# Kernel optimization log

Hardware: AMD Instinct MI355X
Metric: run time of the kernel (lower is better)

The kernel has to match this reference:

```python
import jax, jax.numpy as jnp
import numpy as np

EPS_SLOPE = 1e-4
EPS_AVG = 1e-8
MIN_AVG = 1e-6
EPS_SCALE = 1e-3


def _slopes_yk(xk, delta_raw):
    # xk: [D, K] sorted knot x-positions; delta_raw: [D, K-1]
    seg_dx = xk[:, 1:] - xk[:, :-1]                      # [D, K-1]
    slopes = jax.nn.softplus(delta_raw) + EPS_SLOPE       # [D, K-1]
    avg = (slopes * seg_dx).sum(1, keepdims=True) / (seg_dx.sum(1, keepdims=True) + EPS_AVG)
    avg = jnp.maximum(avg, MIN_AVG)
    slopes = slopes / avg
    yk = jnp.concatenate(
        [jnp.zeros((xk.shape[0], 1), dtype=xk.dtype), jnp.cumsum(slopes * seg_dx, axis=1)],
        axis=1,
    )                                                     # [D, K]
    return slopes, yk


def setup_inputs() -> dict:
    key = jax.random.key(0)
    k1, k2, k3, k4, k5 = jax.random.split(key, 5)
    N, D, K = 1_000_000, 64, 32
    x = jax.random.normal(k1, (N, D), dtype=jnp.float32)
    # sorted knots per dim, spanning roughly the data range
    xk = jnp.sort(jax.random.normal(k2, (D, K), dtype=jnp.float32) * 2.0, axis=1)
    delta_raw = jax.random.normal(k3, (D, K - 1), dtype=jnp.float32) * 0.1
    scale_raw = jax.random.normal(k4, (D,), dtype=jnp.float32) * 0.1
    shift = jax.random.normal(k5, (D,), dtype=jnp.float32) * 0.1
    return {"x": x, "xk": xk, "delta_raw": delta_raw, "scale_raw": scale_raw, "shift": shift}


def reference(x, xk, delta_raw, scale_raw, shift):
    # x: [N, D]; xk: [D, K]
    D, K = xk.shape
    slopes, yk = _slopes_yk(xk, delta_raw)
    xT = x.T                                              # [D, N]
    # per-dim binary search (torch.searchsorted default == side='left')
    idx = jax.vmap(lambda knots, vals: jnp.searchsorted(knots, vals))(xk, xT)
    i0 = jnp.clip(idx, 1, K - 1) - 1                      # [D, N]
    x0 = jnp.take_along_axis(xk, i0, axis=1)              # [D, N]
    y0 = jnp.take_along_axis(yk, i0, axis=1)
    m = jnp.take_along_axis(slopes, i0, axis=1)
    y = (y0 + m * (xT - x0)).T                            # [N, D]
    scale = jax.nn.softplus(scale_raw) + EPS_SCALE
    return y * scale + shift
```

## Files before the change

### kernel.cpp

```cpp
#include <hip/hip_runtime.h>
#include <math.h>

#define D 64
#define KNOTS 32
#define NSEG 31
#define G 512
#define TSTR 66

typedef float f2v __attribute__((ext_vector_type(2)));

__device__ __forceinline__ float softplus_f(float v) {
  return fmaxf(v, 0.f) + log1pf(expf(-fabsf(v)));
}

__global__ __launch_bounds__(1024, 8) void pwl_fused(
    const float* __restrict__ x, const float* __restrict__ xk,
    const float* __restrict__ delta_raw, const float* __restrict__ scale_raw,
    const float* __restrict__ shift, float* __restrict__ out, int nrows) {
  __shared__ float kL[KNOTS * D];
  __shared__ float2 sAB[NSEG * D];
  __shared__ unsigned char tab[G * TSTR];
  __shared__ float invS[D], nloS[D];

  const int tid = threadIdx.x;

  for (int i = tid; i < D * KNOTS; i += blockDim.x) {
    int d = i >> 5, j = i & 31;
    int sd = (d >> 1) | ((d & 1) << 5);
    kL[j * D + sd] = xk[i];
  }
  __syncthreads();

  if (tid < D) {
    const int sd = tid;
    const int d = ((sd & 31) << 1) | (sd >> 5);
    float num = 0.f, den = 0.f;
    for (int s = 0; s < NSEG; ++s) {
      float sp = softplus_f(delta_raw[d * NSEG + s]) + 1e-4f;
      float dx = kL[(s + 1) * D + sd] - kL[s * D + sd];
      num += sp * dx;
      den += dx;
    }
    float avg = fmaxf(num / (den + 1e-8f), 1e-6f);
    float scale = softplus_f(scale_raw[d]) + 1e-3f;
    float sh = shift[d];
    float y = 0.f;
    for (int s = 0; s < NSEG; ++s) {
      float sp = softplus_f(delta_raw[d * NSEG + s]) + 1e-4f;
      float m = sp / avg;
      float k0 = kL[s * D + sd];
      sAB[s * D + sd] = make_float2(m * scale, (y - m * k0) * scale + sh);
      y += m * (kL[(s + 1) * D + sd] - k0);
    }
    float lo = kL[1 * D + sd];
    float hi = kL[(KNOTS - 1) * D + sd];
    float inv = (float)G / (hi - lo);
    invS[sd] = inv;
    nloS[sd] = -lo * inv;
  }
  __syncthreads();

  for (int p = tid; p < G * D; p += blockDim.x) {
    const int sd = p & 63;
    const int c = p >> 6;
    const float inv = invS[sd], nlo = nloS[sd];
    int b = 0;
#pragma unroll
    for (int half = 16; half > 0; half >>= 1) {
      float kv = kL[(b + half) * D + sd];
      float cf = fminf(fmaxf(fmaf(kv, inv, nlo), 0.f), (float)(G - 1));
      b += ((int)cf < c) ? half : 0;
    }
    tab[c * TSTR + sd] = (unsigned char)min(b, 30);
  }
  __syncthreads();

  const int lane = tid & 63;
  const int m = lane & 31;
  const int sd0 = m;
  const int sd1 = 32 + m;
  const float inv0 = invS[sd0], nlo0 = nloS[sd0];
  const float inv1 = invS[sd1], nlo1 = nloS[sd1];

  const f2v* __restrict__ x2 = (const f2v*)x;
  f2v* __restrict__ o2 = (f2v*)out;

  auto evalpair = [&](f2v xv) -> f2v {
    float cf0 = fminf(fmaxf(fmaf(xv.x, inv0, nlo0), 0.f), (float)(G - 1));
    float cf1 = fminf(fmaxf(fmaf(xv.y, inv1, nlo1), 0.f), (float)(G - 1));
    int c0 = (int)cf0, c1 = (int)cf1;
    int i0 = tab[c0 * TSTR + sd0];
    int i1 = tab[c1 * TSTR + sd1];
    float2 a0 = sAB[i0 * D + sd0];
    float2 a1 = sAB[i1 * D + sd1];
    f2v r;
    r.x = fmaf(a0.x, xv.x, a0.y);
    r.y = fmaf(a1.x, xv.y, a1.y);
    return r;
  };

  const int gwave = (int)(blockIdx.x * blockDim.x + tid) >> 6;
  const int nwave = (int)(gridDim.x * blockDim.x) >> 6;
  const int ngroups = nrows >> 4;

  for (int g = gwave; g < ngroups; g += nwave) {
    const int base = g * 512 + lane;
    f2v v0 = x2[base];
    f2v v1 = x2[base + 64];
    f2v v2 = x2[base + 128];
    f2v v3 = x2[base + 192];
    f2v v4 = x2[base + 256];
    f2v v5 = x2[base + 320];
    f2v v6 = x2[base + 384];
    f2v v7 = x2[base + 448];

    f2v r0 = evalpair(v0);
    f2v r1 = evalpair(v1);
    f2v r2 = evalpair(v2);
    f2v r3 = evalpair(v3);
    f2v r4 = evalpair(v4);
    f2v r5 = evalpair(v5);
    f2v r6 = evalpair(v6);
    f2v r7 = evalpair(v7);

    __builtin_nontemporal_store(r0, &o2[base]);
    __builtin_nontemporal_store(r1, &o2[base + 64]);
    __builtin_nontemporal_store(r2, &o2[base + 128]);
    __builtin_nontemporal_store(r3, &o2[base + 192]);
    __builtin_nontemporal_store(r4, &o2[base + 256]);
    __builtin_nontemporal_store(r5, &o2[base + 320]);
    __builtin_nontemporal_store(r6, &o2[base + 384]);
    __builtin_nontemporal_store(r7, &o2[base + 448]);
  }

  for (int r = (ngroups << 4) + gwave; r < nrows; r += nwave) {
    if (lane < 32) {
      const int bi = r * 32 + m;
      f2v xv = x2[bi];
      f2v rv = evalpair(xv);
      __builtin_nontemporal_store(rv, &o2[bi]);
    }
  }
}

extern "C" void kernel_launch(void* const* d_in, const int* in_sizes, int n_in,
                              void* d_out, int out_size, void* d_ws, size_t ws_size,
                              hipStream_t stream) {
  const float* x = (const float*)d_in[0];
  const float* xk = (const float*)d_in[1];
  const float* delta_raw = (const float*)d_in[2];
  const float* scale_raw = (const float*)d_in[3];
  const float* shift = (const float*)d_in[4];
  float* out = (float*)d_out;

  const int nrows = in_sizes[0] / D;
  const int block = 1024;
  const int grid = 512;
  pwl_fused<<<grid, block, 0, stream>>>(x, xk, delta_raw, scale_raw, shift,
                                        out, nrows);
}
```

Measured before the change: 119.3 us.

## Double-buffer row-group loads with contiguous per-wave chunks

Each wave now gets a contiguous chunk of row groups instead of a grid-strided set. Within that chunk the loads are software-pipelined in two register sets, so the next group's global loads are issued before the current group is evaluated and stored. The goal is to hide memory latency in this bandwidth-bound kernel. The cost is roughly 16 more live vector registers per thread, which could lower occupancy at 1024 threads per block, and the contiguous per-wave chunks change the DRAM access pattern across the grid.

```diff
diff --git a/kernel.cpp b/kernel.cpp
--- a/kernel.cpp
+++ b/kernel.cpp
@@ -102,38 +102,63 @@
   const int gwave = (int)(blockIdx.x * blockDim.x + tid) >> 6;
   const int nwave = (int)(gridDim.x * blockDim.x) >> 6;
   const int ngroups = nrows >> 4;
+  const int chunk = (ngroups + nwave - 1) / nwave;
+  int g = gwave * chunk;
+  const int gend = min(g + chunk, ngroups);
 
-  for (int g = gwave; g < ngroups; g += nwave) {
-    const int base = g * 512 + lane;
-    f2v v0 = x2[base];
-    f2v v1 = x2[base + 64];
-    f2v v2 = x2[base + 128];
-    f2v v3 = x2[base + 192];
-    f2v v4 = x2[base + 256];
-    f2v v5 = x2[base + 320];
-    f2v v6 = x2[base + 384];
-    f2v v7 = x2[base + 448];
+  f2v a0, a1, a2, a3, a4, a5, a6, a7;
+  f2v b0, b1, b2, b3, b4, b5, b6, b7;
 
-    f2v r0 = evalpair(v0);
-    f2v r1 = evalpair(v1);
-    f2v r2 = evalpair(v2);
-    f2v r3 = evalpair(v3);
-    f2v r4 = evalpair(v4);
-    f2v r5 = evalpair(v5);
-    f2v r6 = evalpair(v6);
-    f2v r7 = evalpair(v7);
-
-    __builtin_nontemporal_store(r0, &o2[base]);
-    __builtin_nontemporal_store(r1, &o2[base + 64]);
-    __builtin_nontemporal_store(r2, &o2[base + 128]);
-    __builtin_nontemporal_store(r3, &o2[base + 192]);
-    __builtin_nontemporal_store(r4, &o2[base + 256]);
-    __builtin_nontemporal_store(r5, &o2[base + 320]);
-    __builtin_nontemporal_store(r6, &o2[base + 384]);
-    __builtin_nontemporal_store(r7, &o2[base + 448]);
+#define LOADG(p, gg)                                                   \
+  {                                                                    \
+    const int base_ = (gg) * 512 + lane;                               \
+    p##0 = x2[base_];        p##1 = x2[base_ + 64];                    \
+    p##2 = x2[base_ + 128];  p##3 = x2[base_ + 192];                   \
+    p##4 = x2[base_ + 256];  p##5 = x2[base_ + 320];                   \
+    p##6 = x2[base_ + 384];  p##7 = x2[base_ + 448];                   \
   }
 
-  for (int r = (ngroups << 4) + gwave; r < nrows; r += nwave) {
+#define PROCG(p, gg)                                                   \
+  {                                                                    \
+    const int base_ = (gg) * 512 + lane;                               \
+    f2v r_;                                                            \
+    r_ = evalpair(p##0); __builtin_nontemporal_store(r_, &o2[base_]);       \
+    r_ = evalpair(p##1); __builtin_nontemporal_store(r_, &o2[base_ + 64]);  \
+    r_ = evalpair(p##2); __builtin_nontemporal_store(r_, &o2[base_ + 128]); \
+    r_ = evalpair(p##3); __builtin_nontemporal_store(r_, &o2[base_ + 192]); \
+    r_ = evalpair(p##4); __builtin_nontemporal_store(r_, &o2[base_ + 256]); \
+    r_ = evalpair(p##5); __builtin_nontemporal_store(r_, &o2[base_ + 320]); \
+    r_ = evalpair(p##6); __builtin_nontemporal_store(r_, &o2[base_ + 384]); \
+    r_ = evalpair(p##7); __builtin_nontemporal_store(r_, &o2[base_ + 448]); \
+  }
+
+  if (g < gend) {
+    LOADG(a, g);
+    while (true) {
+      const int gn = g + 1;
+      if (gn < gend) {
+        LOADG(b, gn);
+        PROCG(a, g);
+        const int gnn = gn + 1;
+        if (gnn < gend) {
+          LOADG(a, gnn);
+          PROCG(b, gn);
+          g = gnn;
+        } else {
+          PROCG(b, gn);
+          break;
+        }
+      } else {
+        PROCG(a, g);
+        break;
+      }
+    }
+  }
+#undef LOADG
+#undef PROCG
+
+  const int tg0 = ngroups << 4;
+  for (int r = tg0 + gwave; r < nrows; r += nwave) {
     if (lane < 32) {
       const int bi = r * 32 + m;
       f2v xv = x2[bi];
```

Result: faster. 112.7 us (-5.5%).
